# Performance work log

Measured on AMD Instinct MI355X. Metric: run time of the kernel, lower is better.

The kernel has to match this reference:

```python
import jax, jax.numpy as jnp
import numpy as np

B = 65536      # batch
C = 1000       # num_classes
D = 256        # feat_dim


def _l2norm(x, eps=1e-12):
    # matches F.normalize(dim=1): v / max(||v||_2, eps)
    n = jnp.linalg.norm(x, axis=1, keepdims=True)
    return x / jnp.maximum(n, eps)


def setup_inputs() -> dict:
    key = jax.random.key(0)
    k1, k2, k3, k4, k5 = jax.random.split(key, 5)
    bound = 1.0 / np.sqrt(D)
    X = jax.random.normal(k1, (B, D), dtype=jnp.float32)
    labels = jax.random.randint(k2, (B,), 0, C)
    signatures = jax.random.uniform(k3, (C, D), dtype=jnp.float32, minval=-bound, maxval=bound)
    b_means = jax.random.uniform(k4, (1, D), dtype=jnp.float32, minval=-bound, maxval=bound)
    b_covs = jax.random.normal(k5, (D, D), dtype=jnp.float32)
    return {"X": X, "labels": labels, "signatures": signatures,
            "b_means": b_means, "b_covs": b_covs}


def reference(X, labels, signatures, b_means, b_covs):
    # SVD-based whitening of background covariance (tiny DxD)
    cov = b_covs @ b_covs.T
    U, eig, _ = jnp.linalg.svd(cov)
    DU = (eig ** -0.5)[:, None] * U.T              # diag(eig^-1/2) @ U^T, [D, D]
    xHat = _l2norm((X - b_means) @ DU.T)           # [B, D]
    sHat = _l2norm(signatures @ DU.T)              # [C, D]
    ACE_targets = xHat @ sHat.T                    # [B, C] cosine scores
    labels = labels.astype(jnp.int32)
    numerator = jnp.take_along_axis(ACE_targets, labels[:, None], axis=1)[:, 0]
    # denominator = exp(true) + sum(exp(others)) == sum over all classes
    loss = -jnp.mean(numerator - jax.nn.logsumexp(ACE_targets, axis=1))
    return (loss, ACE_targets)
```

## Files before the change

### kernel.cpp

```cpp
#include <hip/hip_runtime.h>
#include <hip/hip_bf16.h>
#include <math.h>

#define D_ 256
#define B_ 65536
#define C_ 1000

typedef _Float16 f16x8 __attribute__((ext_vector_type(8)));
typedef float f32x4 __attribute__((ext_vector_type(4)));

__global__ void transpose_kernel(const float* __restrict__ in, float* __restrict__ out,
                                 double* __restrict__ acc) {
  __shared__ float t[32][33];
  if (blockIdx.x == 0 && threadIdx.x == 0) *acc = 0.0;
  const int bx = blockIdx.x & 7, by = blockIdx.x >> 3;
  const int lx = threadIdx.x & 31, ly = threadIdx.x >> 5;
#pragma unroll
  for (int s = 0; s < 4; ++s) {
    int r = by * 32 + ly + s * 8;
    t[ly + s * 8][lx] = in[r * 256 + bx * 32 + lx];
  }
  __syncthreads();
#pragma unroll
  for (int s = 0; s < 4; ++s) {
    int r = bx * 32 + ly + s * 8;
    out[r * 256 + by * 32 + lx] = t[lx][ly + s * 8];
  }
}

__global__ void cov_kernel(const float* __restrict__ bc, const float* __restrict__ bcT,
                           double* __restrict__ C64) {
  const int i = blockIdx.x, j = threadIdx.x;
  __shared__ float ri[D_];
  ri[j] = bc[i * D_ + j];
  __syncthreads();
  double s = 0.0;
#pragma unroll 8
  for (int k = 0; k < D_; ++k) s += (double)ri[k] * (double)bcT[k * D_ + j];
  C64[i * D_ + j] = s;
}

__global__ __launch_bounds__(256, 1) void chol_panel(double* __restrict__ A, int p) {
  const int j0 = p * 64;
  const int r = threadIdx.x;
  __shared__ double rowv[64];
  __shared__ double dinv;
  double pr[64];
  const bool act = (r >= j0);
  if (act) {
#pragma unroll
    for (int k = 0; k < 64; ++k) pr[k] = A[(size_t)r * D_ + j0 + k];
  }
#pragma unroll
  for (int j = 0; j < 64; ++j) {
    const int col = j0 + j;
    if (r == col) { double d = sqrt(pr[j]); pr[j] = d; dinv = 1.0 / d; }
    __syncthreads();
    if (r > col) {
      double lr = pr[j] * dinv;
      pr[j] = lr;
      if (r < j0 + 64) rowv[r - j0] = lr;
    }
    __syncthreads();
    if (r > col) {
      const double lr = pr[j];
#pragma unroll
      for (int k = j + 1; k < 64; ++k) pr[k] -= lr * rowv[k];
    }
  }
  if (act) {
    const int kmax = (r - j0 < 63) ? (r - j0) : 63;
#pragma unroll
    for (int k = 0; k < 64; ++k)
      if (k <= kmax) A[(size_t)r * D_ + j0 + k] = pr[k];
  }
}

__global__ __launch_bounds__(256) void chol_trail(double* __restrict__ A, int p) {
  const int j0 = p * 64;
  const int t0 = j0 + 64;
  int b = blockIdx.x, I = 0;
  while (b >= I + 1) { b -= I + 1; ++I; }
  const int J = b;
  const int r0 = t0 + I * 64, c0 = t0 + J * 64;
  __shared__ double LR[64][67];
  __shared__ double LC[64][67];
  const int tid = threadIdx.x;
  for (int e = tid; e < 64 * 64; e += 256) {
    int rr = e >> 6, cc = e & 63;
    LR[rr][cc] = A[(size_t)(r0 + rr) * D_ + j0 + cc];
    LC[rr][cc] = A[(size_t)(c0 + rr) * D_ + j0 + cc];
  }
  __syncthreads();
  const int tx = tid & 15, ty = tid >> 4;
  double acc[4][4];
#pragma unroll
  for (int i = 0; i < 4; ++i)
#pragma unroll
    for (int j = 0; j < 4; ++j) acc[i][j] = 0.0;
#pragma unroll 4
  for (int k = 0; k < 64; ++k) {
    double a_[4], b_[4];
#pragma unroll
    for (int i = 0; i < 4; ++i) a_[i] = LR[ty + 16 * i][k];
#pragma unroll
    for (int j = 0; j < 4; ++j) b_[j] = LC[tx + 16 * j][k];
#pragma unroll
    for (int i = 0; i < 4; ++i)
#pragma unroll
      for (int j = 0; j < 4; ++j) acc[i][j] += a_[i] * b_[j];
  }
#pragma unroll
  for (int i = 0; i < 4; ++i) {
    const int grow = r0 + ty + 16 * i;
#pragma unroll
    for (int j = 0; j < 4; ++j) {
      const int gcol = c0 + tx + 16 * j;
      A[(size_t)grow * D_ + gcol] -= acc[i][j];
    }
  }
}

__global__ __launch_bounds__(256) void inv_kernel(const double* __restrict__ L,
                                                  _Float16* __restrict__ WbP,
                                                  _Float16* __restrict__ WbT) {
  const int c = blockIdx.x;
  const int tid = threadIdx.x;
  __shared__ double w[D_];
  __shared__ double rdi[D_];
  __shared__ double rhs[32];
  __shared__ double Ldd[32][33];
  w[tid] = 0.0;
  rdi[tid] = 1.0 / L[(size_t)tid * D_ + tid];
  __syncthreads();
  const int q0 = c >> 5;
  for (int q = q0; q < 8; ++q) {
    const int i0 = q * 32;
    const int ii = tid >> 3, s = tid & 7;
    const int i = i0 + ii;
    double part = 0.0;
    for (int k = c + s; k < i0; k += 8) part += L[(size_t)i * D_ + k] * w[k];
    part += __shfl_xor(part, 1, 64);
    part += __shfl_xor(part, 2, 64);
    part += __shfl_xor(part, 4, 64);
    if (s == 0) rhs[ii] = ((i == c) ? 1.0 : 0.0) - part;
    for (int e = tid; e < 32 * 32; e += 256) {
      int rr = e >> 5, cc = e & 31;
      Ldd[rr][cc] = L[(size_t)(i0 + rr) * D_ + i0 + cc];
    }
    __syncthreads();
    if (tid < 32) {
      double x = rhs[tid];
      double v = 0.0;
      for (int j = 0; j < 32; ++j) {
        double xj = __shfl(x, j, 64);
        double wj = xj * rdi[i0 + j];
        if (tid == j) v = wj;
        if (tid > j) x -= Ldd[tid][j] * wj;
      }
      w[i0 + tid] = v;
    }
    __syncthreads();
  }
  _Float16 h = (_Float16)(float)w[tid];
  WbT[(size_t)c * D_ + tid] = h;
  {
    const int g = tid >> 4, lrr = tid & 15;
    const int ks = c >> 5, lqq = (c >> 3) & 3, jj = c & 7;
    WbP[(size_t)(g * 8 + ks) * 512 + (size_t)(lqq * 16 + lrr) * 8 + jj] = h;
  }
}

__global__ void sig_kernel(const float* __restrict__ S, const _Float16* __restrict__ WbT,
                           _Float16* __restrict__ sHatP) {
  int c = blockIdx.x, i = threadIdx.x;
  const int g = c >> 4, lr = c & 15;
  const int ks = i >> 5, lq = (i >> 3) & 3, jj = i & 7;
  const size_t off = (size_t)(g * 8 + ks) * 512 + (size_t)(lq * 16 + lr) * 8 + jj;
  if (c >= C_) { sHatP[off] = (_Float16)0.0f; return; }
  __shared__ float srow[D_];
  __shared__ float wred[4];
  srow[i] = S[c * D_ + i];
  __syncthreads();
  float t = 0.f;
  for (int k = 0; k < D_; ++k) t += (float)WbT[k * D_ + i] * srow[k];
  float ss = t * t;
#pragma unroll
  for (int d = 1; d < 64; d <<= 1) ss += __shfl_xor(ss, d, 64);
  if ((i & 63) == 0) wred[i >> 6] = ss;
  __syncthreads();
  float tot = wred[0] + wred[1] + wred[2] + wred[3];
  float rn = 1.0f / fmaxf(sqrtf(tot), 1e-12f);
  sHatP[off] = (_Float16)(t * rn);
}

__global__ __launch_bounds__(512) void xform_kernel(const float* __restrict__ X,
                                                    const float* __restrict__ means,
                                                    const _Float16* __restrict__ WbP,
                                                    _Float16* __restrict__ xHat,
                                                    float* __restrict__ rnX) {
  __shared__ __align__(16) _Float16 Wsh[65536];
  __shared__ float msh[D_];
  const int tid = threadIdx.x;
  const int wid = tid >> 6, l = tid & 63, lr = l & 15, lq = l >> 4;
  const int rowbase = blockIdx.x * 128;
  const int arow = rowbase + wid * 16 + lr;
  if (tid < 256) msh[tid] = means[tid];
#pragma unroll
  for (int s = 0; s < 16; ++s) {
    const int off = (wid * 16 + s) * 512;
    __builtin_amdgcn_global_load_lds(
        (const __attribute__((address_space(1))) unsigned int*)(WbP + off + l * 8),
        (__attribute__((address_space(3))) unsigned int*)(&Wsh[off]), 16, 0, 0);
  }
  __syncthreads();

  f16x8 af[8];
#pragma unroll
  for (int ks = 0; ks < 8; ++ks) {
    const float* xp = X + (size_t)arow * D_ + lq * 8 + ks * 32;
    const float4 x0 = *(const float4*)(xp);
    const float4 x1 = *(const float4*)(xp + 4);
    const int mb = lq * 8 + ks * 32;
    af[ks][0] = (_Float16)(x0.x - msh[mb + 0]);
    af[ks][1] = (_Float16)(x0.y - msh[mb + 1]);
    af[ks][2] = (_Float16)(x0.z - msh[mb + 2]);
    af[ks][3] = (_Float16)(x0.w - msh[mb + 3]);
    af[ks][4] = (_Float16)(x1.x - msh[mb + 4]);
    af[ks][5] = (_Float16)(x1.y - msh[mb + 5]);
    af[ks][6] = (_Float16)(x1.z - msh[mb + 6]);
    af[ks][7] = (_Float16)(x1.w - msh[mb + 7]);
  }

  float ss[4] = {0.f, 0.f, 0.f, 0.f};
  const _Float16* bb = &Wsh[(size_t)l * 8];
  for (int ch = 0; ch < 2; ++ch) {
    f32x4 acc[8];
#pragma unroll
    for (int t = 0; t < 8; ++t) acc[t] = (f32x4){0.f, 0.f, 0.f, 0.f};
#pragma unroll
    for (int ks = 0; ks < 8; ++ks) {
#pragma unroll
      for (int t = 0; t < 8; ++t) {
        f16x8 bf = *(const f16x8*)(bb + (ch * 64 + t * 8 + ks) * 512);
        acc[t] = __builtin_amdgcn_mfma_f32_16x16x32_f16(af[ks], bf, acc[t], 0, 0, 0);
      }
    }
#pragma unroll
    for (int t = 0; t < 8; ++t) {
      const int col = ch * 128 + t * 16 + lr;
#pragma unroll
      for (int j = 0; j < 4; ++j) {
        const int row = rowbase + wid * 16 + lq * 4 + j;
        float v = acc[t][j];
        ss[j] += v * v;
        xHat[(size_t)row * D_ + col] = (_Float16)v;
      }
    }
  }
#pragma unroll
  for (int d = 1; d < 16; d <<= 1) {
#pragma unroll
    for (int j = 0; j < 4; ++j) ss[j] += __shfl_xor(ss[j], d, 64);
  }
  if (lr == 0) {
#pragma unroll
    for (int j = 0; j < 4; ++j) {
      const int row = rowbase + wid * 16 + lq * 4 + j;
      rnX[row] = 1.0f / fmaxf(sqrtf(ss[j]), 1e-12f);
    }
  }
}

__global__ __launch_bounds__(512) void ace_kernel(const _Float16* __restrict__ xHat,
                                                  const _Float16* __restrict__ sHatP,
                                                  const float* __restrict__ rnX,
                                                  const int* __restrict__ labels,
                                                  float* __restrict__ outACE,
                                                  double* __restrict__ acc_loss) {
  __shared__ __align__(16) _Float16 Bsh[2][64 * 512];
  __shared__ float part[32];
  const int tid = threadIdx.x;
  const int wid = tid >> 6, l = tid & 63, lr = l & 15, lq = l >> 4;
  const int rowbase = blockIdx.x * 128;
  const int wrow = rowbase + wid * 16;

  f16x8 a[8];
  {
    const _Float16* ap = xHat + (size_t)(wrow + lr) * D_ + lq * 8;
#pragma unroll
    for (int ks = 0; ks < 8; ++ks) a[ks] = *(const f16x8*)(ap + ks * 32);
  }

  int lab[4]; float rx[4], ssum[4], num[4];
#pragma unroll
  for (int j = 0; j < 4; ++j) {
    int row = wrow + lq * 4 + j;
    lab[j] = labels[row];
    rx[j] = rnX[row];
    ssum[j] = 0.f; num[j] = 0.f;
  }

#define STAGE(bufi, chi) do {                                                        \
    const _Float16* _src = sHatP + (size_t)(chi) * 32768;                            \
    _Float16* _dst = &Bsh[bufi][0];                                                  \
    _Pragma("unroll")                                                                \
    for (int _s = 0; _s < 8; ++_s) {                                                 \
      const int _off = wid * 4096 + _s * 512;                                        \
      __builtin_amdgcn_global_load_lds(                                              \
          (const __attribute__((address_space(1))) unsigned int*)(_src + _off + l * 8), \
          (__attribute__((address_space(3))) unsigned int*)(_dst + _off), 16, 0, 0); \
    } } while (0)

  float* const outrow = outACE + (size_t)(wrow + lq * 4) * C_;

  STAGE(0, 0);
  __syncthreads();
  int buf = 0;
  for (int ch = 0; ch < 8; ++ch) {
    if (ch < 7) {
      STAGE(buf ^ 1, ch + 1);
      __builtin_amdgcn_sched_barrier(0);
    }
    const _Float16* bb = &Bsh[buf][(size_t)l * 8];
    f32x4 acc[8];
#pragma unroll
    for (int t = 0; t < 8; ++t) acc[t] = (f32x4){0.f, 0.f, 0.f, 0.f};
#pragma unroll
    for (int ks = 0; ks < 8; ++ks) {
#pragma unroll
      for (int t = 0; t < 8; ++t) {
        f16x8 bf = *(const f16x8*)(bb + (t * 8 + ks) * 512);
        acc[t] = __builtin_amdgcn_mfma_f32_16x16x32_f16(a[ks], bf, acc[t], 0, 0, 0);
      }
    }
#pragma unroll
    for (int t = 0; t < 8; ++t) {
      const int col = ch * 128 + t * 16 + lr;
      const bool valid = (col < C_);
#pragma unroll
      for (int j = 0; j < 4; ++j) {
        float v = acc[t][j] * rx[j];
        if (valid) outrow[(size_t)j * C_ + col] = v;
        ssum[j] += __expf(v - 1.0f);
        num[j] = (col == lab[j]) ? v : num[j];
      }
    }
    if (ch < 7) {
      __builtin_amdgcn_sched_barrier(0);
      asm volatile("s_waitcnt vmcnt(32)" ::: "memory");
      __builtin_amdgcn_s_barrier();
      __builtin_amdgcn_sched_barrier(0);
    }
    buf ^= 1;
  }
#undef STAGE

#pragma unroll
  for (int d2 = 1; d2 < 16; d2 <<= 1) {
#pragma unroll
    for (int j = 0; j < 4; ++j) {
      ssum[j] += __shfl_xor(ssum[j], d2, 64);
      num[j]  += __shfl_xor(num[j], d2, 64);
    }
  }
  if (lr == 0) {
    const float padcorr = 24.0f * __expf(-1.0f);
    float contrib = 0.f;
#pragma unroll
    for (int j = 0; j < 4; ++j)
      contrib += num[j] - (1.0f + __logf(ssum[j] - padcorr));
    part[wid * 4 + lq] = contrib;
  }
  __syncthreads();
  if (tid == 0) {
    float s = 0.f;
#pragma unroll
    for (int p2 = 0; p2 < 32; ++p2) s += part[p2];
    atomicAdd(acc_loss, (double)s);
  }
}

__global__ void fin_kernel(const double* a, float* out) {
  out[0] = (float)(-(*a) / (double)B_);
}

extern "C" void kernel_launch(void* const* d_in, const int* in_sizes, int n_in,
                              void* d_out, int out_size, void* d_ws, size_t ws_size,
                              hipStream_t stream) {
  const float* X      = (const float*)d_in[0];
  const int*   labels = (const int*)d_in[1];
  const float* S      = (const float*)d_in[2];
  const float* means  = (const float*)d_in[3];
  const float* bc     = (const float*)d_in[4];
  float* out = (float*)d_out;

  char* w = (char*)d_ws;
  double*    acc   = (double*)(w + 0);
  double*    C64   = (double*)(w + 256);
  _Float16*  WbP   = (_Float16*)(w + 524544);
  _Float16*  WbT   = (_Float16*)(w + 655616);
  _Float16*  sHatP = (_Float16*)(w + 786688);
  float*     rnX   = (float*)(w + 1310976);
  _Float16*  xHat  = (_Float16*)(w + 1573120);
  float*     bcT   = (float*)(w + 1573120);

  transpose_kernel<<<64, 256, 0, stream>>>(bc, bcT, acc);
  cov_kernel<<<256, 256, 0, stream>>>(bc, bcT, C64);
  for (int p = 0; p < 4; ++p) {
    chol_panel<<<1, 256, 0, stream>>>(C64, p);
    int nt = 3 - p;
    if (nt > 0) chol_trail<<<nt * (nt + 1) / 2, 256, 0, stream>>>(C64, p);
  }
  inv_kernel<<<256, 256, 0, stream>>>(C64, WbP, WbT);
  sig_kernel<<<1024, 256, 0, stream>>>(S, WbT, sHatP);
  xform_kernel<<<512, 512, 0, stream>>>(X, means, WbP, xHat, rnX);
  ace_kernel<<<512, 512, 0, stream>>>(xHat, sHatP, rnX, labels, out + 1, acc);
  fin_kernel<<<1, 1, 0, stream>>>(acc, out);
}
```

Before: 372.0 us.

## Fuse transpose into tiled cov, halve panel syncs, widen ACE blocks

Drops the separate transpose kernel by having a 32x32-tiled cov kernel read both operands straight from the input, which saves one launch. The Cholesky panel now computes the pivot's reciprocal square root redundantly in every thread, using a float rsqrt refined by two Newton steps, and double-buffers the pivot row, so each column needs one barrier instead of two. The ACE kernel moves to 1024-thread blocks covering 256 rows, so each staged signature chunk is shared by twice as many waves. In exchange, the rsqrt-plus-Newton path may differ slightly from an exact sqrt, and the larger blocks reduce scheduling flexibility.

```diff
diff --git a/kernel.cpp b/kernel.cpp
--- a/kernel.cpp
+++ b/kernel.cpp
@@ -9,64 +9,68 @@
 typedef _Float16 f16x8 __attribute__((ext_vector_type(8)));
 typedef float f32x4 __attribute__((ext_vector_type(4)));
 
-__global__ void transpose_kernel(const float* __restrict__ in, float* __restrict__ out,
-                                 double* __restrict__ acc) {
-  __shared__ float t[32][33];
-  if (blockIdx.x == 0 && threadIdx.x == 0) *acc = 0.0;
-  const int bx = blockIdx.x & 7, by = blockIdx.x >> 3;
-  const int lx = threadIdx.x & 31, ly = threadIdx.x >> 5;
-#pragma unroll
-  for (int s = 0; s < 4; ++s) {
-    int r = by * 32 + ly + s * 8;
-    t[ly + s * 8][lx] = in[r * 256 + bx * 32 + lx];
-  }
-  __syncthreads();
-#pragma unroll
-  for (int s = 0; s < 4; ++s) {
-    int r = bx * 32 + ly + s * 8;
-    out[r * 256 + by * 32 + lx] = t[lx][ly + s * 8];
-  }
-}
-
-__global__ void cov_kernel(const float* __restrict__ bc, const float* __restrict__ bcT,
-                           double* __restrict__ C64) {
-  const int i = blockIdx.x, j = threadIdx.x;
-  __shared__ float ri[D_];
-  ri[j] = bc[i * D_ + j];
-  __syncthreads();
-  double s = 0.0;
+__global__ __launch_bounds__(256) void cov_kernel(const float* __restrict__ bc,
+                                                  double* __restrict__ C64,
+                                                  double* __restrict__ acc) {
+  __shared__ float Ash[32][260];
+  __shared__ float Bsh2[32][260];
+  const int b = blockIdx.x, bi = b >> 3, bj = b & 7;
+  const int e = threadIdx.x;
+  if (b == 0 && e == 0) *acc = 0.0;
+#pragma unroll
+  for (int s = 0; s < 32; ++s) {
+    int lin = s * 256 + e;
+    int rr = lin >> 8, cc = lin & 255;
+    Ash[rr][cc] = bc[(bi * 32 + rr) * 256 + cc];
+    Bsh2[rr][cc] = bc[(bj * 32 + rr) * 256 + cc];
+  }
+  __syncthreads();
+  const int tx = e & 15, ty = e >> 4;
+  double a00 = 0, a01 = 0, a10 = 0, a11 = 0;
 #pragma unroll 8
-  for (int k = 0; k < D_; ++k) s += (double)ri[k] * (double)bcT[k * D_ + j];
-  C64[i * D_ + j] = s;
+  for (int k = 0; k < 256; ++k) {
+    double ar0 = (double)Ash[ty][k], ar1 = (double)Ash[ty + 16][k];
+    double br0 = (double)Bsh2[tx][k], br1 = (double)Bsh2[tx + 16][k];
+    a00 += ar0 * br0; a01 += ar0 * br1;
+    a10 += ar1 * br0; a11 += ar1 * br1;
+  }
+  const int r0 = bi * 32, c0 = bj * 32;
+  C64[(size_t)(r0 + ty) * D_ + c0 + tx] = a00;
+  C64[(size_t)(r0 + ty) * D_ + c0 + tx + 16] = a01;
+  C64[(size_t)(r0 + ty + 16) * D_ + c0 + tx] = a10;
+  C64[(size_t)(r0 + ty + 16) * D_ + c0 + tx + 16] = a11;
 }
 
 __global__ __launch_bounds__(256, 1) void chol_panel(double* __restrict__ A, int p) {
   const int j0 = p * 64;
   const int r = threadIdx.x;
-  __shared__ double rowv[64];
-  __shared__ double dinv;
+  __shared__ double raw[2][64];
   double pr[64];
   const bool act = (r >= j0);
+  const bool inpanel = act && (r < j0 + 64);
   if (act) {
 #pragma unroll
     for (int k = 0; k < 64; ++k) pr[k] = A[(size_t)r * D_ + j0 + k];
   }
+  if (inpanel) raw[0][r - j0] = pr[0];
+  __syncthreads();
 #pragma unroll
   for (int j = 0; j < 64; ++j) {
     const int col = j0 + j;
-    if (r == col) { double d = sqrt(pr[j]); pr[j] = d; dinv = 1.0 / d; }
+    const double d2 = raw[j & 1][j];
+    double rs = (double)rsqrtf((float)d2);
+    rs = rs * (1.5 - 0.5 * d2 * rs * rs);
+    rs = rs * (1.5 - 0.5 * d2 * rs * rs);
+    if (r >= col) {
+      const double lr_ = pr[j] * rs;
+      pr[j] = lr_;
+#pragma unroll
+      for (int k = j + 1; k < 64; ++k) pr[k] -= lr_ * (raw[j & 1][k] * rs);
+    }
+    if (j < 63) {
+      if (r > col && r < j0 + 64) raw[(j + 1) & 1][r - j0] = pr[j + 1];
+    }
     __syncthreads();
-    if (r > col) {
-      double lr = pr[j] * dinv;
-      pr[j] = lr;
-      if (r < j0 + 64) rowv[r - j0] = lr;
-    }
-    __syncthreads();
-    if (r > col) {
-      const double lr = pr[j];
-#pragma unroll
-      for (int k = j + 1; k < 64; ++k) pr[k] -= lr * rowv[k];
-    }
   }
   if (act) {
     const int kmax = (r - j0 < 63) ? (r - j0) : 63;
@@ -272,17 +276,17 @@
   }
 }
 
-__global__ __launch_bounds__(512) void ace_kernel(const _Float16* __restrict__ xHat,
-                                                  const _Float16* __restrict__ sHatP,
-                                                  const float* __restrict__ rnX,
-                                                  const int* __restrict__ labels,
-                                                  float* __restrict__ outACE,
-                                                  double* __restrict__ acc_loss) {
+__global__ __launch_bounds__(1024) void ace_kernel(const _Float16* __restrict__ xHat,
+                                                   const _Float16* __restrict__ sHatP,
+                                                   const float* __restrict__ rnX,
+                                                   const int* __restrict__ labels,
+                                                   float* __restrict__ outACE,
+                                                   double* __restrict__ acc_loss) {
   __shared__ __align__(16) _Float16 Bsh[2][64 * 512];
-  __shared__ float part[32];
+  __shared__ float part[64];
   const int tid = threadIdx.x;
   const int wid = tid >> 6, l = tid & 63, lr = l & 15, lq = l >> 4;
-  const int rowbase = blockIdx.x * 128;
+  const int rowbase = blockIdx.x * 256;
   const int wrow = rowbase + wid * 16;
 
   f16x8 a[8];
@@ -305,8 +309,8 @@
     const _Float16* _src = sHatP + (size_t)(chi) * 32768;                            \
     _Float16* _dst = &Bsh[bufi][0];                                                  \
     _Pragma("unroll")                                                                \
-    for (int _s = 0; _s < 8; ++_s) {                                                 \
-      const int _off = wid * 4096 + _s * 512;                                        \
+    for (int _s = 0; _s < 4; ++_s) {                                                 \
+      const int _off = wid * 2048 + _s * 512;                                        \
       __builtin_amdgcn_global_load_lds(                                              \
           (const __attribute__((address_space(1))) unsigned int*)(_src + _off + l * 8), \
           (__attribute__((address_space(3))) unsigned int*)(_dst + _off), 16, 0, 0); \
@@ -376,7 +380,7 @@
   if (tid == 0) {
     float s = 0.f;
 #pragma unroll
-    for (int p2 = 0; p2 < 32; ++p2) s += part[p2];
+    for (int p2 = 0; p2 < 64; ++p2) s += part[p2];
     atomicAdd(acc_loss, (double)s);
   }
 }
@@ -403,10 +407,8 @@
   _Float16*  sHatP = (_Float16*)(w + 786688);
   float*     rnX   = (float*)(w + 1310976);
   _Float16*  xHat  = (_Float16*)(w + 1573120);
-  float*     bcT   = (float*)(w + 1573120);
-
-  transpose_kernel<<<64, 256, 0, stream>>>(bc, bcT, acc);
-  cov_kernel<<<256, 256, 0, stream>>>(bc, bcT, C64);
+
+  cov_kernel<<<64, 256, 0, stream>>>(bc, C64, acc);
   for (int p = 0; p < 4; ++p) {
     chol_panel<<<1, 256, 0, stream>>>(C64, p);
     int nt = 3 - p;
@@ -415,6 +417,6 @@
   inv_kernel<<<256, 256, 0, stream>>>(C64, WbP, WbT);
   sig_kernel<<<1024, 256, 0, stream>>>(S, WbT, sHatP);
   xform_kernel<<<512, 512, 0, stream>>>(X, means, WbP, xHat, rnX);
-  ace_kernel<<<512, 512, 0, stream>>>(xHat, sHatP, rnX, labels, out + 1, acc);
+  ace_kernel<<<256, 1024, 0, stream>>>(xHat, sHatP, rnX, labels, out + 1, acc);
   fin_kernel<<<1, 1, 0, stream>>>(acc, out);
 }
```

After: 367.5 us. Within noise of the previous version (-1.2%).
